# Kernel tuning notes

Measured on AMD Instinct MI355X. Metric: run time of the kernel, lower is better.

The kernel has to match this reference:

```python
import jax, jax.numpy as jnp
import numpy as np

B, L, H = 2, 2048, 1536
I, N, R, K = 3072, 16, 96, 4


def setup_inputs() -> dict:
    key = jax.random.key(0)
    ks = jax.random.split(key, 10)
    rn = lambda k, shape, s: jax.random.normal(k, shape, jnp.float32) * s
    return {
        "hidden_states": rn(ks[0], (B, L, H), 1.0),
        "W_in": rn(ks[1], (2 * I, H), 0.02),
        "conv_w": rn(ks[2], (I, K), 0.1),
        "conv_b": rn(ks[3], (I,), 0.1),
        "W_x": rn(ks[4], (R + 2 * N, I), 0.02),
        "W_dt": rn(ks[5], (I, R), 0.02),
        "dt_bias": rn(ks[6], (I,), 0.1),
        # vLLM's weight loader stores A = -exp(A_log); replicate that here
        "A": -jnp.exp(rn(ks[7], (I, N), 0.5)),
        "D": jnp.ones((I,), jnp.float32),
        "W_out": rn(ks[8], (H, I), 0.02),
    }


def reference(hidden_states, W_in, conv_w, conv_b, W_x, W_dt, dt_bias, A, D, W_out):
    b, l, _ = hidden_states.shape
    k = conv_w.shape[1]
    n = A.shape[1]
    r = W_dt.shape[1]

    # in_proj -> [B,L,2I], split into ssm input x and gate
    proj = jnp.einsum("blh,eh->ble", hidden_states, W_in)
    x, gate = jnp.split(proj, 2, axis=-1)  # each [B,L,I]

    # causal depthwise conv1d over L (pad K-1 on the left) + SiLU
    xp = jnp.pad(x, ((0, 0), (k - 1, 0), (0, 0)))
    conv = sum(xp[:, j : j + l, :] * conv_w[:, j] for j in range(k)) + conv_b
    x = jax.nn.silu(conv)  # [B,L,I]

    # x_proj -> dt (rank R), B, C (each N)
    ssm_p = jnp.einsum("bli,pi->blp", x, W_x)
    dt_in, Bm, Cm = jnp.split(ssm_p, [r, r + n], axis=-1)

    # dt_proj (skip_bias_add) then softplus(dt + bias) inside the scan math
    dt = jnp.einsum("blr,ir->bli", dt_in, W_dt)
    delta = jax.nn.softplus(dt + dt_bias)  # [B,L,I]

    # selective scan: s_t = exp(delta_t * A) * s_{t-1} + delta_t * x_t * B_t
    def step(state, inp):
        d_t, u_t, B_t, C_t = inp  # [B,I], [B,I], [B,N], [B,N]
        dA = jnp.exp(d_t[..., None] * A)  # [B,I,N]
        state = state * dA + (d_t * u_t)[..., None] * B_t[:, None, :]
        y = jnp.einsum("bin,bn->bi", state, C_t)
        return state, y

    init = jnp.zeros((b, x.shape[-1], n), jnp.float32)
    _, ys = jax.lax.scan(
        step,
        init,
        (
            delta.transpose(1, 0, 2),
            x.transpose(1, 0, 2),
            Bm.transpose(1, 0, 2),
            Cm.transpose(1, 0, 2),
        ),
    )
    y = ys.transpose(1, 0, 2) + x * D  # skip connection via D
    y = y * jax.nn.silu(gate)

    # out_proj -> [B,L,H]
    return jnp.einsum("bli,hi->blh", y, W_out)
```

## Files before the change

### kernel.cpp

```cpp
#include <hip/hip_runtime.h>

typedef __attribute__((ext_vector_type(8))) short bf16x8;
typedef __attribute__((ext_vector_type(4))) float f32x4;

#define CCH 32
#define TCH 64

__device__ __forceinline__ unsigned short f2b(float f) {
    unsigned u = __float_as_uint(f);
    return (unsigned short)((u + 0x7fffu + ((u >> 16) & 1u)) >> 16);
}
__device__ __forceinline__ float b2f(unsigned short h) {
    return __uint_as_float(((unsigned)h) << 16);
}
__device__ __forceinline__ float softplus_f(float z) {
    return (z > 15.f) ? z : __logf(1.f + __expf(z));
}
__device__ __forceinline__ float silu_f(float g) {
    return g / (1.f + __expf(-g));
}

__device__ __forceinline__ void gload16(const unsigned short* g, unsigned short* l) {
    __builtin_amdgcn_global_load_lds(
        (const __attribute__((address_space(1))) void*)g,
        (__attribute__((address_space(3))) void*)l, 16, 0, 0);
}

__global__ __launch_bounds__(256)
void cast_all(const float* __restrict__ h, const float* __restrict__ win,
              const float* __restrict__ wx, const float* __restrict__ wdt,
              const float* __restrict__ wout,
              unsigned short* __restrict__ dh, unsigned short* __restrict__ dwin,
              unsigned short* __restrict__ dwx, unsigned short* __restrict__ dwdt,
              unsigned short* __restrict__ dwout) {
    const int n0 = 1572864, n1 = n0 + 2359296, n2 = n1 + 98304,
              n3 = n2 + 73728, n4 = n3 + 1179648;
    int i = blockIdx.x * 256 + threadIdx.x;
    const float* s; unsigned short* d; int off;
    if (i < n0)      { s = h;    d = dh;    off = i; }
    else if (i < n1) { s = win;  d = dwin;  off = i - n0; }
    else if (i < n2) { s = wx;   d = dwx;   off = i - n1; }
    else if (i < n3) { s = wdt;  d = dwdt;  off = i - n2; }
    else if (i < n4) { s = wout; d = dwout; off = i - n3; }
    else return;
    float4 v = reinterpret_cast<const float4*>(s)[off];
    ushort4 o;
    o.x = f2b(v.x); o.y = f2b(v.y); o.z = f2b(v.z); o.w = f2b(v.w);
    reinterpret_cast<ushort4*>(d)[off] = o;
}

template <int OP>
__global__ __launch_bounds__(256)
void gemm_mfma(const unsigned short* __restrict__ A, const unsigned short* __restrict__ W,
               void* __restrict__ Cout, int Kc, int lda, int ldw, int ldc,
               const float* __restrict__ bias, int silu_col0, long long czs) {
    __shared__ unsigned short As[3][4096];
    __shared__ unsigned short Bs[3][4096];
    const int tid = threadIdx.x;
    const int bm = blockIdx.y * 128;
    const int bn = blockIdx.x * 128;
    const int kz = blockIdx.z;
    A += (size_t)kz * Kc;
    W += (size_t)kz * Kc;
    const int lane = tid & 63;
    const int wave = tid >> 6;
    const int r_a = lane >> 2;
    const int k8 = (lane & 3) * 8;

    const unsigned short* gA0 = A + (size_t)(bm + wave * 16 + r_a) * lda + k8;
    const unsigned short* gA1 = A + (size_t)(bm + 64 + wave * 16 + r_a) * lda + k8;
    const unsigned short* gB0 = W + (size_t)(bn + wave * 16 + r_a) * ldw + k8;
    const unsigned short* gB1 = W + (size_t)(bn + 64 + wave * 16 + r_a) * ldw + k8;

    const int wm = (wave & 1) * 64;
    const int wn = (wave >> 1) * 64;
    const int lr = lane & 15;
    const int quad = lane >> 4;

    f32x4 acc[4][4];
    const f32x4 zero = {0.f, 0.f, 0.f, 0.f};
#pragma unroll
    for (int i = 0; i < 4; i++)
#pragma unroll
        for (int j = 0; j < 4; j++) acc[i][j] = zero;

#define STAGE(koff, j) do { \
        gload16(gA0 + (koff), As[j] + wave * 512); \
        gload16(gA1 + (koff), As[j] + (wave + 4) * 512); \
        gload16(gB0 + (koff), Bs[j] + wave * 512); \
        gload16(gB1 + (koff), Bs[j] + (wave + 4) * 512); \
    } while (0)

    const int niter = Kc >> 5;
    STAGE(0, 0);
    if (niter > 1) STAGE(32, 1);

    int ib = 0;
    for (int k = 0; k < niter; k++) {
        if (k + 1 < niter)
            asm volatile("s_waitcnt vmcnt(4)\n\ts_barrier" ::: "memory");
        else
            asm volatile("s_waitcnt vmcnt(0)\n\ts_barrier" ::: "memory");
        if (k + 2 < niter) {
            int is_ = ib + 2; if (is_ >= 3) is_ -= 3;
            STAGE((k + 2) << 5, is_);
        }
        const unsigned short* as = As[ib];
        const unsigned short* bs = Bs[ib];
        bf16x8 fa[4], fb[4];
#pragma unroll
        for (int mi = 0; mi < 4; mi++)
            fa[mi] = *reinterpret_cast<const bf16x8*>(as + (wm + mi * 16 + lr) * 32 + quad * 8);
#pragma unroll
        for (int ni = 0; ni < 4; ni++)
            fb[ni] = *reinterpret_cast<const bf16x8*>(bs + (wn + ni * 16 + lr) * 32 + quad * 8);
#pragma unroll
        for (int mi = 0; mi < 4; mi++)
#pragma unroll
            for (int ni = 0; ni < 4; ni++)
                acc[mi][ni] = __builtin_amdgcn_mfma_f32_16x16x32_bf16(fa[mi], fb[ni], acc[mi][ni], 0, 0, 0);
        ib = (ib == 2) ? 0 : ib + 1;
    }
#undef STAGE

#pragma unroll
    for (int mi = 0; mi < 4; mi++)
#pragma unroll
        for (int reg = 0; reg < 4; reg++) {
            int row = bm + wm + mi * 16 + quad * 4 + reg;
#pragma unroll
            for (int ni = 0; ni < 4; ni++) {
                int col = bn + wn + ni * 16 + lr;
                float v = acc[mi][ni][reg];
                if (OP == 0) {
                    float* Cf = (float*)Cout + (size_t)kz * czs;
                    Cf[(size_t)row * ldc + col] = v;
                } else if (OP == 2) {
                    if (col >= silu_col0) v = silu_f(v);
                    ((unsigned short*)Cout)[(size_t)row * ldc + col] = f2b(v);
                } else {
                    ((unsigned short*)Cout)[(size_t)row * ldc + col] = f2b(softplus_f(v + bias[col]));
                }
            }
        }
}

__global__ __launch_bounds__(256)
void reduce_out(const float* __restrict__ p, float* __restrict__ out, int n4) {
    int i = blockIdx.x * 256 + threadIdx.x;
    if (i >= n4) return;
    float4 a = reinterpret_cast<const float4*>(p)[i];
    float4 b = reinterpret_cast<const float4*>(p + (size_t)n4 * 4)[i];
    float4 o = {a.x + b.x, a.y + b.y, a.z + b.z, a.w + b.w};
    reinterpret_cast<float4*>(out)[i] = o;
}

__global__ __launch_bounds__(256)
void reduce_xpart(const float* __restrict__ xpart, float* __restrict__ ssmp,
                  unsigned short* __restrict__ dtin) {
    const int BL = 4096;
    int idx = blockIdx.x * 256 + threadIdx.x;
    int row = idx >> 5;
    int c4 = (idx & 31) * 4;
    float4 s = {0.f, 0.f, 0.f, 0.f};
#pragma unroll
    for (int z = 0; z < 8; z++) {
        float4 v = *reinterpret_cast<const float4*>(xpart + (size_t)z * BL * 128 + (size_t)row * 128 + c4);
        s.x += v.x; s.y += v.y; s.z += v.z; s.w += v.w;
    }
    *reinterpret_cast<float4*>(ssmp + (size_t)row * 128 + c4) = s;
    if (c4 < 96) {
        ushort4 o;
        o.x = f2b(s.x); o.y = f2b(s.y); o.z = f2b(s.z); o.w = f2b(s.w);
        *reinterpret_cast<ushort4*>(dtin + (size_t)row * 96 + c4) = o;
    }
}

__global__ __launch_bounds__(256)
void conv_silu8(const unsigned short* __restrict__ projbf, const float* __restrict__ cw,
                const float* __restrict__ cb, unsigned short* __restrict__ xc) {
    const int I = 3072, L = 2048, LD = 6144;
    int idx = blockIdx.x * 256 + threadIdx.x;
    int i8 = (idx % (I / 8)) * 8;
    int bl = idx / (I / 8);
    int l = bl & (L - 1);
    float s[8];
    {
        float4 b0 = *reinterpret_cast<const float4*>(cb + i8);
        float4 b1 = *reinterpret_cast<const float4*>(cb + i8 + 4);
        s[0]=b0.x; s[1]=b0.y; s[2]=b0.z; s[3]=b0.w; s[4]=b1.x; s[5]=b1.y; s[6]=b1.z; s[7]=b1.w;
    }
    float w[8][4];
#pragma unroll
    for (int c = 0; c < 8; c++) {
        float4 wr = *reinterpret_cast<const float4*>(cw + (i8 + c) * 4);
        w[c][0]=wr.x; w[c][1]=wr.y; w[c][2]=wr.z; w[c][3]=wr.w;
    }
#pragma unroll
    for (int j = 0; j < 4; j++) {
        if (l + j - 3 >= 0) {
            uint4 r = *reinterpret_cast<const uint4*>(projbf + (size_t)(bl + j - 3) * LD + i8);
            float xv[8];
            xv[0]=b2f((unsigned short)(r.x & 0xffff)); xv[1]=b2f((unsigned short)(r.x >> 16));
            xv[2]=b2f((unsigned short)(r.y & 0xffff)); xv[3]=b2f((unsigned short)(r.y >> 16));
            xv[4]=b2f((unsigned short)(r.z & 0xffff)); xv[5]=b2f((unsigned short)(r.z >> 16));
            xv[6]=b2f((unsigned short)(r.w & 0xffff)); xv[7]=b2f((unsigned short)(r.w >> 16));
#pragma unroll
            for (int c = 0; c < 8; c++) s[c] = fmaf(xv[c], w[c][j], s[c]);
        }
    }
    unsigned short o[8];
#pragma unroll
    for (int c = 0; c < 8; c++) o[c] = f2b(silu_f(s[c]));
    uint4 packed;
    packed.x = (unsigned)o[0] | ((unsigned)o[1] << 16);
    packed.y = (unsigned)o[2] | ((unsigned)o[3] << 16);
    packed.z = (unsigned)o[4] | ((unsigned)o[5] << 16);
    packed.w = (unsigned)o[6] | ((unsigned)o[7] << 16);
    *reinterpret_cast<uint4*>(xc + (size_t)bl * I + i8) = packed;
}

__global__ __launch_bounds__(256)
void scan_passA(const unsigned short* __restrict__ delta_bf, const unsigned short* __restrict__ xc,
                const float* __restrict__ ssmp, const float* __restrict__ Aw,
                float* __restrict__ S_local, float* __restrict__ sumDelta) {
    const int I = 3072, L = 2048;
    __shared__ float bc[TCH][32];
    int g = blockIdx.x * 256 + threadIdx.x;
    int i = g % I;
    int bcid = g / I;
    int c = bcid % CCH;
    int b = bcid / CCH;
    size_t rowbase = (size_t)b * L + (size_t)c * TCH;
    for (int e = threadIdx.x; e < TCH * 8; e += 256) {
        int t = e >> 3, q = e & 7;
        float4 v = *reinterpret_cast<const float4*>(ssmp + (rowbase + t) * 128 + 96 + q * 4);
        *reinterpret_cast<float4*>(&bc[t][q * 4]) = v;
    }
    __syncthreads();

    float Arow[16];
#pragma unroll
    for (int n = 0; n < 16; n++) Arow[n] = Aw[i * 16 + n];
    float st[16];
#pragma unroll
    for (int n = 0; n < 16; n++) st[n] = 0.f;
    float sumD = 0.f;

    size_t rowI = rowbase * I + i;
    for (int t = 0; t < TCH; t++) {
        float delta = b2f(delta_bf[rowI]);
        float du = delta * b2f(xc[rowI]);
        sumD += delta;
        float4 b0 = *reinterpret_cast<const float4*>(&bc[t][0]);
        float4 b1 = *reinterpret_cast<const float4*>(&bc[t][4]);
        float4 b2 = *reinterpret_cast<const float4*>(&bc[t][8]);
        float4 b3 = *reinterpret_cast<const float4*>(&bc[t][12]);
        const float bv[16] = {b0.x,b0.y,b0.z,b0.w, b1.x,b1.y,b1.z,b1.w,
                              b2.x,b2.y,b2.z,b2.w, b3.x,b3.y,b3.z,b3.w};
#pragma unroll
        for (int n = 0; n < 16; n++)
            st[n] = fmaf(st[n], __expf(delta * Arow[n]), du * bv[n]);
        rowI += I;
    }
    size_t obase = (size_t)bcid * 16 * I + i;
#pragma unroll
    for (int n = 0; n < 16; n++) S_local[obase + (size_t)n * I] = st[n];
    sumDelta[(size_t)bcid * I + i] = sumD;
}

__global__ __launch_bounds__(256)
void scan_passB(const float* __restrict__ S_local, const float* __restrict__ sumDelta,
                const float* __restrict__ Aw, float* __restrict__ state_in) {
    const int I = 3072;
    int g = blockIdx.x * 256 + threadIdx.x;
    int i = g % I;
    int bn = g / I;
    int n = bn & 15;
    int b = bn >> 4;
    float a = Aw[i * 16 + n];
    float state = 0.f;
    for (int c = 0; c < CCH; c++) {
        int bcid = b * CCH + c;
        size_t idx = ((size_t)bcid * 16 + n) * I + i;
        state_in[idx] = state;
        state = fmaf(state, __expf(a * sumDelta[(size_t)bcid * I + i]), S_local[idx]);
    }
}

__global__ __launch_bounds__(256)
void scan_passC(const unsigned short* __restrict__ projbf,
                const unsigned short* __restrict__ xc,
                const float* __restrict__ ssmp, const unsigned short* __restrict__ delta_bf,
                const float* __restrict__ Aw, const float* __restrict__ Dw,
                const float* __restrict__ state_in, unsigned short* __restrict__ ybf) {
    const int I = 3072, L = 2048, LD = 6144;
    __shared__ float bc[TCH][32];
    int g = blockIdx.x * 256 + threadIdx.x;
    int i = g % I;
    int bcid = g / I;
    int c = bcid % CCH;
    int b = bcid / CCH;
    size_t rowbase = (size_t)b * L + (size_t)c * TCH;
    for (int e = threadIdx.x; e < TCH * 8; e += 256) {
        int t = e >> 3, q = e & 7;
        float4 v = *reinterpret_cast<const float4*>(ssmp + (rowbase + t) * 128 + 96 + q * 4);
        *reinterpret_cast<float4*>(&bc[t][q * 4]) = v;
    }
    __syncthreads();

    float Arow[16];
#pragma unroll
    for (int n = 0; n < 16; n++) Arow[n] = Aw[i * 16 + n];
    float Dv = Dw[i];
    float st[16];
    size_t sbase = (size_t)bcid * 16 * I + i;
#pragma unroll
    for (int n = 0; n < 16; n++) st[n] = state_in[sbase + (size_t)n * I];

    size_t rowI = rowbase * I + i;
    size_t rowG = rowbase * LD + I + i;
    for (int t = 0; t < TCH; t++) {
        float delta = b2f(delta_bf[rowI]);
        float u = b2f(xc[rowI]);
        float du = delta * u;
        float4 b0 = *reinterpret_cast<const float4*>(&bc[t][0]);
        float4 b1 = *reinterpret_cast<const float4*>(&bc[t][4]);
        float4 b2 = *reinterpret_cast<const float4*>(&bc[t][8]);
        float4 b3 = *reinterpret_cast<const float4*>(&bc[t][12]);
        float4 c0 = *reinterpret_cast<const float4*>(&bc[t][16]);
        float4 c1 = *reinterpret_cast<const float4*>(&bc[t][20]);
        float4 c2 = *reinterpret_cast<const float4*>(&bc[t][24]);
        float4 c3 = *reinterpret_cast<const float4*>(&bc[t][28]);
        const float bv[16] = {b0.x,b0.y,b0.z,b0.w, b1.x,b1.y,b1.z,b1.w,
                              b2.x,b2.y,b2.z,b2.w, b3.x,b3.y,b3.z,b3.w};
        const float cv[16] = {c0.x,c0.y,c0.z,c0.w, c1.x,c1.y,c1.z,c1.w,
                              c2.x,c2.y,c2.z,c2.w, c3.x,c3.y,c3.z,c3.w};
        float y = 0.f;
#pragma unroll
        for (int n = 0; n < 16; n++) {
            st[n] = fmaf(st[n], __expf(delta * Arow[n]), du * bv[n]);
            y = fmaf(st[n], cv[n], y);
        }
        y = fmaf(u, Dv, y);
        y *= b2f(projbf[rowG]);
        ybf[rowI] = f2b(y);
        rowI += I;
        rowG += LD;
    }
}

extern "C" void kernel_launch(void* const* d_in, const int* in_sizes, int n_in,
                              void* d_out, int out_size, void* d_ws, size_t ws_size,
                              hipStream_t stream) {
    const float* hidden  = (const float*)d_in[0];
    const float* W_in    = (const float*)d_in[1];
    const float* conv_w  = (const float*)d_in[2];
    const float* conv_b  = (const float*)d_in[3];
    const float* W_x     = (const float*)d_in[4];
    const float* W_dt    = (const float*)d_in[5];
    const float* dt_bias = (const float*)d_in[6];
    const float* Aw      = (const float*)d_in[7];
    const float* Dw      = (const float*)d_in[8];
    const float* W_out   = (const float*)d_in[9];
    float* out = (float*)d_out;

    constexpr int Bsz = 2, L = 2048, H = 1536, I = 3072, R = 96;
    constexpr int BL = Bsz * L;
    constexpr int TwoI = 2 * I;

    char* base = (char*)d_ws;
    unsigned short* proj_bf  = (unsigned short*)base; base += (size_t)BL * TwoI * 2;
    unsigned short* delta_bf = (unsigned short*)base; base += (size_t)BL * I * 2;
    unsigned short* xc_bf    = (unsigned short*)base; base += (size_t)BL * I * 2;
    unsigned short* y_bf     = (unsigned short*)base; base += (size_t)BL * I * 2;
    float* ssmp              = (float*)base;          base += (size_t)BL * 128 * 4;
    float* xpart             = (float*)base;          base += (size_t)8 * BL * 128 * 4;
    unsigned short* dtin_bf  = (unsigned short*)base; base += (size_t)BL * R * 2;
    unsigned short* wx_bf    = (unsigned short*)base; base += (size_t)128 * I * 2;
    unsigned short* wdt_bf   = (unsigned short*)base; base += (size_t)I * R * 2;
    unsigned short* wout_bf  = (unsigned short*)base; base += (size_t)H * I * 2;
    unsigned short* h_bf     = (unsigned short*)base; base += (size_t)BL * H * 2;
    unsigned short* win_bf   = (unsigned short*)base; base += (size_t)TwoI * H * 2;
    float* S_local  = (float*)h_bf;
    float* sumDelta = S_local + (size_t)Bsz * CCH * 16 * I;
    float* state_in = sumDelta + (size_t)Bsz * CCH * I;
    float* opart = (float*)proj_bf;

    dim3 blk(256);

    cast_all<<<(5283840 + 255) / 256, blk, 0, stream>>>(
        hidden, W_in, W_x, W_dt, W_out, h_bf, win_bf, wx_bf, wdt_bf, wout_bf);

    gemm_mfma<2><<<dim3(TwoI / 128, BL / 128, 1), blk, 0, stream>>>(
        h_bf, win_bf, proj_bf, H, H, H, TwoI, nullptr, I, 0);

    conv_silu8<<<BL * I / 8 / 256, blk, 0, stream>>>(proj_bf, conv_w, conv_b, xc_bf);

    gemm_mfma<0><<<dim3(1, BL / 128, 8), blk, 0, stream>>>(
        xc_bf, wx_bf, xpart, I / 8, I, I, 128, nullptr, 0, (long long)BL * 128);
    reduce_xpart<<<BL * 32 / 256, blk, 0, stream>>>(xpart, ssmp, dtin_bf);

    gemm_mfma<3><<<dim3(I / 128, BL / 128, 1), blk, 0, stream>>>(
        dtin_bf, wdt_bf, delta_bf, R, R, R, I, dt_bias, 0, 0);

    scan_passA<<<Bsz * I * CCH / 256, blk, 0, stream>>>(
        delta_bf, xc_bf, ssmp, Aw, S_local, sumDelta);
    scan_passB<<<Bsz * 16 * I / 256, blk, 0, stream>>>(
        S_local, sumDelta, Aw, state_in);
    scan_passC<<<Bsz * I * CCH / 256, blk, 0, stream>>>(
        proj_bf, xc_bf, ssmp, delta_bf, Aw, Dw, state_in, y_bf);

    gemm_mfma<0><<<dim3(H / 128, BL / 128, 2), blk, 0, stream>>>(
        y_bf, wout_bf, opart, I / 2, I, I, H, nullptr, 0, (long long)BL * H);
    reduce_out<<<BL * H / 4 / 256, blk, 0, stream>>>(opart, out, BL * H / 4);
}
```

Measured before the change: 478.5 us.

## Add 256x256-tile 8-wave MFMA GEMM for in_proj and out_proj

Introduces a new GEMM kernel using 256x256 output tiles with 512 threads, XOR-swizzled LDS staging via global_load_lds, a double-buffered ping-pong schedule with explicit barriers, waitcnt and setprio, and an XCD-aware block remapping. The in_proj and out_proj GEMMs now use it in place of the 128x128 kernel. The aim is more data reuse per tile and overlap of loads with MFMA work. The cost is far fewer workgroups (384 and 192) on a 256-CU part, 128KB of LDS per block, and high register pressure.

```diff
diff --git a/kernel.cpp b/kernel.cpp
--- a/kernel.cpp
+++ b/kernel.cpp
@@ -50,6 +50,161 @@
 }
 
 template <int OP>
+__global__ __launch_bounds__(512)
+void gemm256(const unsigned short* __restrict__ A, const unsigned short* __restrict__ W,
+             void* __restrict__ Cout, int Kc, int lda, int ldw, int ldc,
+             int ntx, int silu_col0, long long czs) {
+    __shared__ __align__(16) unsigned short lds[65536];
+    const int tid  = threadIdx.x;
+    const int lane = tid & 63;
+    const int wave = tid >> 6;
+    const int wr   = wave >> 2;
+    const int wc   = wave & 3;
+    const int lr   = lane & 15;
+    const int quad = lane >> 4;
+    const int sw   = lr & 7;
+
+    const int nwg = gridDim.x;
+    const int wg  = blockIdx.x;
+    const int wgs = (wg & 7) * (nwg >> 3) + (wg >> 3);
+    const int bm  = (wgs / ntx) * 256;
+    const int bn  = (wgs % ntx) * 256;
+    const int kz  = blockIdx.z;
+    A += (size_t)kz * Kc;
+    W += (size_t)kz * Kc;
+
+    const int rsub = wave * 8 + (lane >> 3);
+    const int csw  = ((lane & 7) ^ ((lane >> 3) & 7)) * 8;
+    const unsigned short* gA = A + (size_t)(bm + rsub) * lda + csw;
+    const unsigned short* gB = W + (size_t)(bn + rsub) * ldw + csw;
+
+#define STA(b, h, kt) do { \
+        gload16(gA + (size_t)((h) * 128) * lda + (kt) * 64,      &lds[(b) * 16384 + (h) * 8192 + wave * 512]); \
+        gload16(gA + (size_t)((h) * 128 + 64) * lda + (kt) * 64, &lds[(b) * 16384 + (h) * 8192 + 4096 + wave * 512]); \
+    } while (0)
+#define STB(b, h, kt) do { \
+        gload16(gB + (size_t)((h) * 128) * ldw + (kt) * 64,      &lds[32768 + (b) * 16384 + (h) * 8192 + wave * 512]); \
+        gload16(gB + (size_t)((h) * 128 + 64) * ldw + (kt) * 64, &lds[32768 + (b) * 16384 + (h) * 8192 + 4096 + wave * 512]); \
+    } while (0)
+
+#define LDA_F(b, mh, mi, kk) \
+    (*reinterpret_cast<const bf16x8*>(&lds[(b) * 16384 + ((mh) * 128 + wr * 64 + (mi) * 16 + lr) * 64 + (((((kk) << 2) | quad)) ^ sw) * 8]))
+#define LDB_F(b, nh, ni, kk) \
+    (*reinterpret_cast<const bf16x8*>(&lds[32768 + (b) * 16384 + ((nh) * 128 + wc * 32 + (ni) * 16 + lr) * 64 + (((((kk) << 2) | quad)) ^ sw) * 8]))
+
+#define RD_A(b, mh) do { \
+        _Pragma("unroll") for (int mi = 0; mi < 4; ++mi) { \
+            fa[mi][0] = LDA_F(b, mh, mi, 0); \
+            fa[mi][1] = LDA_F(b, mh, mi, 1); } } while (0)
+#define RD_B(b, nh, dst) do { \
+        _Pragma("unroll") for (int ni = 0; ni < 2; ++ni) { \
+            dst[ni][0] = LDB_F(b, nh, ni, 0); \
+            dst[ni][1] = LDB_F(b, nh, ni, 1); } } while (0)
+
+#define MFMA_Q(mh, nh, bb) do { \
+        _Pragma("unroll") for (int mi = 0; mi < 4; ++mi) \
+        _Pragma("unroll") for (int ni = 0; ni < 2; ++ni) { \
+            acc[(mh) * 4 + mi][(nh) * 2 + ni] = __builtin_amdgcn_mfma_f32_16x16x32_bf16(fa[mi][0], bb[ni][0], acc[(mh) * 4 + mi][(nh) * 2 + ni], 0, 0, 0); \
+            acc[(mh) * 4 + mi][(nh) * 2 + ni] = __builtin_amdgcn_mfma_f32_16x16x32_bf16(fa[mi][1], bb[ni][1], acc[(mh) * 4 + mi][(nh) * 2 + ni], 0, 0, 0); } } while (0)
+
+#define MIDB  asm volatile("s_barrier" ::: "memory")
+#define LGKM0 asm volatile("s_waitcnt lgkmcnt(0)" ::: "memory")
+#define ENDB  asm volatile("s_barrier" ::: "memory")
+#define ENDB_VM4 asm volatile("s_waitcnt vmcnt(4)\n\ts_barrier" ::: "memory")
+#define ENDB_VM0 asm volatile("s_waitcnt vmcnt(0)\n\ts_barrier" ::: "memory")
+#define PRIO1 __builtin_amdgcn_s_setprio(1)
+#define PRIO0 __builtin_amdgcn_s_setprio(0)
+
+    f32x4 acc[8][4];
+    const f32x4 zero = {0.f, 0.f, 0.f, 0.f};
+#pragma unroll
+    for (int m = 0; m < 8; ++m)
+#pragma unroll
+        for (int n = 0; n < 4; ++n) acc[m][n] = zero;
+
+    bf16x8 fa[4][2], fb0[2][2], fb1[2][2];
+
+    const int nkt = Kc >> 6;
+    const int NT2 = nkt >> 1;
+
+    STA(0, 0, 0); STB(0, 0, 0); STA(0, 1, 0); STB(0, 1, 0);
+    STA(1, 0, 1); STB(1, 0, 1);
+    ENDB_VM4;
+
+#pragma unroll 1
+    for (int t = 0; t < NT2 - 1; ++t) {
+        const int k1 = 2 * t + 1, k2 = 2 * t + 2, k3 = 2 * t + 3;
+        RD_A(0, 0); RD_B(0, 0, fb0); STA(1, 1, k1);
+        MIDB; LGKM0; PRIO1; MFMA_Q(0, 0, fb0); PRIO0; ENDB;
+        RD_B(0, 1, fb1); STB(1, 1, k1);
+        MIDB; LGKM0; PRIO1; MFMA_Q(0, 1, fb1); PRIO0; ENDB;
+        RD_A(0, 1); STA(0, 0, k2);
+        MIDB; LGKM0; PRIO1; MFMA_Q(1, 0, fb0); PRIO0; ENDB;
+        STB(0, 0, k2);
+        MIDB; PRIO1; MFMA_Q(1, 1, fb1); PRIO0; ENDB_VM4;
+        RD_A(1, 0); RD_B(1, 0, fb0); STA(0, 1, k2);
+        MIDB; LGKM0; PRIO1; MFMA_Q(0, 0, fb0); PRIO0; ENDB;
+        RD_B(1, 1, fb1); STB(0, 1, k2);
+        MIDB; LGKM0; PRIO1; MFMA_Q(0, 1, fb1); PRIO0; ENDB;
+        RD_A(1, 1); STA(1, 0, k3);
+        MIDB; LGKM0; PRIO1; MFMA_Q(1, 0, fb0); PRIO0; ENDB;
+        STB(1, 0, k3);
+        MIDB; PRIO1; MFMA_Q(1, 1, fb1); PRIO0; ENDB_VM4;
+    }
+    {
+        const int k1 = nkt - 1;
+        RD_A(0, 0); RD_B(0, 0, fb0); STA(1, 1, k1);
+        MIDB; LGKM0; PRIO1; MFMA_Q(0, 0, fb0); PRIO0; ENDB;
+        RD_B(0, 1, fb1); STB(1, 1, k1);
+        MIDB; LGKM0; PRIO1; MFMA_Q(0, 1, fb1); PRIO0; ENDB;
+        RD_A(0, 1);
+        MIDB; LGKM0; PRIO1; MFMA_Q(1, 0, fb0); PRIO0; ENDB;
+        MIDB; PRIO1; MFMA_Q(1, 1, fb1); PRIO0; ENDB_VM0;
+        RD_A(1, 0); RD_B(1, 0, fb0);
+        MIDB; LGKM0; PRIO1; MFMA_Q(0, 0, fb0); PRIO0; ENDB;
+        RD_B(1, 1, fb1);
+        MIDB; LGKM0; PRIO1; MFMA_Q(0, 1, fb1); PRIO0; ENDB;
+        RD_A(1, 1);
+        MIDB; LGKM0; PRIO1; MFMA_Q(1, 0, fb0); PRIO0; ENDB;
+        MIDB; PRIO1; MFMA_Q(1, 1, fb1); PRIO0;
+    }
+
+#pragma unroll
+    for (int m = 0; m < 8; ++m) {
+        const int row0 = bm + (m >> 2) * 128 + wr * 64 + (m & 3) * 16 + quad * 4;
+#pragma unroll
+        for (int n = 0; n < 4; ++n) {
+            const int col = bn + (n >> 1) * 128 + wc * 32 + (n & 1) * 16 + lr;
+#pragma unroll
+            for (int reg = 0; reg < 4; ++reg) {
+                float v = acc[m][n][reg];
+                if (OP == 0) {
+                    float* Cf = (float*)Cout + (size_t)kz * czs;
+                    Cf[(size_t)(row0 + reg) * ldc + col] = v;
+                } else {
+                    if (col >= silu_col0) v = silu_f(v);
+                    ((unsigned short*)Cout)[(size_t)(row0 + reg) * ldc + col] = f2b(v);
+                }
+            }
+        }
+    }
+#undef STA
+#undef STB
+#undef LDA_F
+#undef LDB_F
+#undef RD_A
+#undef RD_B
+#undef MFMA_Q
+#undef MIDB
+#undef LGKM0
+#undef ENDB
+#undef ENDB_VM4
+#undef ENDB_VM0
+#undef PRIO1
+#undef PRIO0
+}
+
+template <int OP>
 __global__ __launch_bounds__(256)
 void gemm_mfma(const unsigned short* __restrict__ A, const unsigned short* __restrict__ W,
                void* __restrict__ Cout, int Kc, int lda, int ldw, int ldc,
@@ -392,8 +547,8 @@
     cast_all<<<(5283840 + 255) / 256, blk, 0, stream>>>(
         hidden, W_in, W_x, W_dt, W_out, h_bf, win_bf, wx_bf, wdt_bf, wout_bf);
 
-    gemm_mfma<2><<<dim3(TwoI / 128, BL / 128, 1), blk, 0, stream>>>(
-        h_bf, win_bf, proj_bf, H, H, H, TwoI, nullptr, I, 0);
+    gemm256<2><<<dim3(24 * 16, 1, 1), dim3(512), 0, stream>>>(
+        h_bf, win_bf, proj_bf, H, H, H, TwoI,  TwoI / 256,  I, 0);
 
     conv_silu8<<<BL * I / 8 / 256, blk, 0, stream>>>(proj_bf, conv_w, conv_b, xc_bf);
 
@@ -411,7 +566,7 @@
     scan_passC<<<Bsz * I * CCH / 256, blk, 0, stream>>>(
         proj_bf, xc_bf, ssmp, delta_bf, Aw, Dw, state_in, y_bf);
 
-    gemm_mfma<0><<<dim3(H / 128, BL / 128, 2), blk, 0, stream>>>(
-        y_bf, wout_bf, opart, I / 2, I, I, H, nullptr, 0, (long long)BL * H);
+    gemm256<0><<<dim3(6 * 16, 1, 2), dim3(512), 0, stream>>>(
+        y_bf, wout_bf, opart, I / 2, I, I, H,  H / 256, 0, (long long)BL * H);
     reduce_out<<<BL * H / 4 / 256, blk, 0, stream>>>(opart, out, BL * H / 4);
 }
```

New measurement: 471.3 us. No clear change (-1.5%).
